# Performance work log

Measured on AMD Instinct MI355X. Metric: run time of the kernel, lower is better.

Reference implementation:

```python
import jax, jax.numpy as jnp
import numpy as np

B, N, F, G = 2, 8, 32, 32
EPS = 1e-8
elu = jax.nn.elu

def pconv(x, w, b):
    # pointwise Conv3d (1x1x1): x (..., C, D, H, W), w (O, C), b (O,)
    return jnp.einsum('...cdhw,oc->...odhw', x, w) + b[:, None, None, None]

def mean_var(x, weight):
    # weighted mean/variance over the num_images axis (axis=1), keepdims
    mean = jnp.sum(x * weight, axis=1, keepdims=True)
    var = jnp.sum(weight * (x - mean) ** 2, axis=1, keepdims=True)
    return mean, var

def setup_inputs() -> dict:
    key = jax.random.key(0)
    ks = jax.random.split(key, 20)
    def wmat(k, o, i):
        return jax.random.normal(k, (o, i), jnp.float32) * (1.0 / np.sqrt(i))
    return {
        'features': jax.random.normal(ks[0], (B, N, F, G, G, G), jnp.float32),
        'mask': jax.random.uniform(ks[1], (B, N, 1, G, G, G), jnp.float32),
        'voxel_depth': jax.random.normal(ks[2], (B, N, 1, G, G, G), jnp.float32),
        'voxel_dir': jax.random.normal(ks[3], (B, N, 3, G, G, G), jnp.float32),
        'rde_w1': wmat(ks[4], F // 2, 4), 'rde_b1': jnp.zeros((F // 2,), jnp.float32),
        'rde_w2': wmat(ks[5], F, F // 2), 'rde_b2': jnp.zeros((F,), jnp.float32),
        'base_w1': wmat(ks[6], 2 * F, 3 * F), 'base_b1': jnp.zeros((2 * F,), jnp.float32),
        'base_w2': wmat(ks[7], F, 2 * F), 'base_b2': jnp.zeros((F,), jnp.float32),
        'vis_w1': wmat(ks[8], F, F), 'vis_b1': jnp.zeros((F,), jnp.float32),
        'vis_w2': wmat(ks[9], F + 1, F), 'vis_b2': jnp.zeros((F + 1,), jnp.float32),
        'vis2_w1': wmat(ks[10], F, F), 'vis2_b1': jnp.zeros((F,), jnp.float32),
        'vis2_w2': wmat(ks[11], 1, F), 'vis2_b2': jnp.zeros((1,), jnp.float32),
        'stat_w': wmat(ks[12], F, 2 * F + 1), 'stat_b': jnp.zeros((F,), jnp.float32),
    }

def reference(features, mask, voxel_depth, voxel_dir,
              rde_w1, rde_b1, rde_w2, rde_b2,
              base_w1, base_b1, base_w2, base_b2,
              vis_w1, vis_b1, vis_w2, vis_b2,
              vis2_w1, vis2_b1, vis2_w2, vis2_b2,
              stat_w, stat_b):
    b, n = features.shape[:2]
    # ray/depth encoder (pointwise MLP over 4 channels)
    rde = jnp.concatenate([voxel_dir, voxel_depth], axis=2)  # (B,N,4,G,G,G)
    rde = elu(pconv(elu(pconv(rde, rde_w1, rde_b1)), rde_w2, rde_b2))
    feats = features + rde
    # mask-normalized weights over views
    weight = mask / (jnp.sum(mask, axis=1, keepdims=True) + EPS)
    mean, var = mean_var(feats, weight)
    gf = jnp.concatenate([mean, var], axis=2)  # (B,1,2F,G,G,G)
    x = jnp.concatenate([jnp.broadcast_to(gf, (b, n) + gf.shape[2:]), feats], axis=2)  # (B,N,3F,...)
    x = elu(pconv(elu(pconv(x, base_w1, base_b1)), base_w2, base_b2))
    xv = elu(pconv(elu(pconv(x * weight, vis_w1, vis_b1)), vis_w2, vis_b2))
    x_res, vis = xv[:, :, :-1], xv[:, :, -1:]
    vis = jax.nn.sigmoid(vis) * mask
    x = x + x_res
    vis = jax.nn.sigmoid(pconv(elu(pconv(x * vis, vis2_w1, vis2_b1)), vis2_w2, vis2_b2)) * mask
    weight = vis / (jnp.sum(vis, axis=1, keepdims=True) + EPS)
    mean, var = mean_var(x, weight)
    gf = jnp.concatenate([mean[:, 0], var[:, 0], jnp.mean(weight, axis=1)], axis=1)  # (B,2F+1,G,G,G)
    return elu(pconv(gf, stat_w, stat_b))  # (B,F,G,G,G)
```

## Files before the change

### kernel.cpp

```cpp
#include <hip/hip_runtime.h>


#define G3 32768
#define KP 104

typedef _Float16 h8 __attribute__((ext_vector_type(8)));
typedef _Float16 h4 __attribute__((ext_vector_type(4)));
typedef float f4 __attribute__((ext_vector_type(4)));

__device__ __forceinline__ float eluf(float x) {
    return x > 0.0f ? x : __expf(x) - 1.0f;
}
__device__ __forceinline__ float sigmoidf(float x) {
    return 1.0f / (1.0f + __expf(-x));
}

#define WS_BW1 0
#define WS_BW2 6144
#define WS_VW1 8192
#define WS_VW2 9216
#define WS_V2W1 10752
#define WS_H_TOT 11776
#define WS_VB2_BYTE (WS_H_TOT * 2)

__global__ void prep_kernel(const float* __restrict__ bw1,
                            const float* __restrict__ bw2,
                            const float* __restrict__ vw1,
                            const float* __restrict__ vw2,
                            const float* __restrict__ v2w1,
                            const float* __restrict__ vb2,
                            _Float16* __restrict__ wh,
                            float* __restrict__ vb2p) {
    int t = blockIdx.x * blockDim.x + threadIdx.x;
    int stride = gridDim.x * blockDim.x;
    for (int i = t; i < 6144; i += stride) wh[WS_BW1 + i] = (_Float16)bw1[i];
    for (int i = t; i < 2048; i += stride) wh[WS_BW2 + i] = (_Float16)bw2[i];
    for (int i = t; i < 1024; i += stride) wh[WS_VW1 + i] = (_Float16)vw1[i];
    for (int i = t; i < 1536; i += stride)
        wh[WS_VW2 + i] = (i < 1056) ? (_Float16)vw2[i] : (_Float16)0.0f;
    for (int i = t; i < 1024; i += stride) wh[WS_V2W1 + i] = (_Float16)v2w1[i];
    for (int i = t; i < 48; i += stride) vb2p[i] = (i < 33) ? vb2[i] : 0.0f;
}

template <int K, int KS, int MT>
__device__ __forceinline__ void mfma_tiles(const _Float16* __restrict__ Wf,
                                           const _Float16* __restrict__ Y,
                                           int srck0, int wave, int lane,
                                           f4 acc[2][4]) {
    const int q = lane >> 4, nlo = lane & 15;
#pragma unroll
    for (int j = 0; j < 2; ++j) {
        const int col = (wave + j * 4) * 16 + nlo;
        const _Float16* yc = Y + col * KP + srck0 + q * 8;
        h8 bf[KS];
#pragma unroll
        for (int kt = 0; kt < KS; ++kt) bf[kt] = *(const h8*)(yc + kt * 32);
#pragma unroll
        for (int mt = 0; mt < MT; ++mt) {
            f4 a = {0.f, 0.f, 0.f, 0.f};
            const _Float16* wr = Wf + (mt * 16 + nlo) * K + q * 8;
#pragma unroll
            for (int kt = 0; kt < KS; ++kt)
                a = __builtin_amdgcn_mfma_f32_16x16x32_f16(
                    *(const h8*)(wr + kt * 32), bf[kt], a, 0, 0, 0);
            acc[j][mt] = a;
        }
    }
}

template <int MT>
__device__ __forceinline__ void epi_store(f4 acc[2][4],
                                          const float* __restrict__ bias,
                                          _Float16* __restrict__ Y, int dstk0,
                                          int wave, int lane) {
    const int q = lane >> 4, nlo = lane & 15;
#pragma unroll
    for (int j = 0; j < 2; ++j) {
        const int col = (wave + j * 4) * 16 + nlo;
#pragma unroll
        for (int mt = 0; mt < MT; ++mt) {
            f4 bb = *(const f4*)(bias + mt * 16 + q * 4);
            f4 v = acc[j][mt];
            h4 hv;
#pragma unroll
            for (int r = 0; r < 4; ++r) hv[r] = (_Float16)eluf(v[r] + bb[r]);
            *(h4*)(Y + col * KP + dstk0 + mt * 16 + q * 4) = hv;
        }
    }
}

__global__ __launch_bounds__(256) void ibr_mfma(
    const float* __restrict__ features, const float* __restrict__ mask,
    const float* __restrict__ vdepth, const float* __restrict__ vdir,
    const float* __restrict__ rde_w1, const float* __restrict__ rde_b1,
    const float* __restrict__ rde_w2, const float* __restrict__ rde_b2,
    const float* __restrict__ base_b1, const float* __restrict__ base_b2,
    const float* __restrict__ vis_b1, const float* __restrict__ vis2_b1,
    const float* __restrict__ vis2_w2, const float* __restrict__ vis2_b2,
    const float* __restrict__ stat_w, const float* __restrict__ stat_b,
    const _Float16* __restrict__ wh, const float* __restrict__ vb2p,
    float* __restrict__ out) {
    __shared__ _Float16 Y[128 * KP];
    __shared__ float wtc[128], mval[128], visn_s[128], visv_s[128], wt2c[128];
    __shared__ float sA_v[16], wm_v[16];

    const int tid = threadIdx.x;
    const int lane = tid & 63;
    const int wave = tid >> 6;
    const int bb = blockIdx.x;
    const int b = bb >> 11;
    const int v0 = (bb & 2047) << 4;

    {
        const int n = tid >> 5, c = tid & 31;
        const float* fp = features + (((b * 8 + n) * 32 + c) << 15) + v0;
        f4 x0 = *(const f4*)(fp);
        f4 x1 = *(const f4*)(fp + 4);
        f4 x2 = *(const f4*)(fp + 8);
        f4 x3 = *(const f4*)(fp + 12);
        float va[16] = {x0[0], x0[1], x0[2], x0[3], x1[0], x1[1], x1[2], x1[3],
                        x2[0], x2[1], x2[2], x2[3], x3[0], x3[1], x3[2], x3[3]};
#pragma unroll
        for (int vi = 0; vi < 16; ++vi)
            Y[(vi * 8 + n) * KP + 64 + c] = (_Float16)va[vi];
    }
    if (tid < 128)
        mval[tid] = mask[((b * 8 + (tid & 7)) << 15) + v0 + (tid >> 3)];
    __syncthreads();

    if (tid < 128) {
        const int n = tid & 7, vi = tid >> 3, col = tid;
        const int bn = b * 8 + n, v = v0 + vi;
        const float r0 = vdir[(bn * 3 + 0) * G3 + v];
        const float r1 = vdir[(bn * 3 + 1) * G3 + v];
        const float r2 = vdir[(bn * 3 + 2) * G3 + v];
        const float r3 = vdepth[bn * G3 + v];
        float h16[16];
#pragma unroll
        for (int o = 0; o < 16; ++o) {
            float a = rde_b1[o] + rde_w1[o * 4 + 0] * r0 +
                      rde_w1[o * 4 + 1] * r1 + rde_w1[o * 4 + 2] * r2 +
                      rde_w1[o * 4 + 3] * r3;
            h16[o] = eluf(a);
        }
        float msum = 0.f;
#pragma unroll
        for (int k = 0; k < 8; ++k) msum += mval[vi * 8 + k];
        const float inv = 1.0f / (msum + 1e-8f);
        wtc[col] = mval[col] * inv;
        if (n == 0) sA_v[vi] = msum * inv;

        _Float16* yc = Y + col * KP + 64;
#pragma unroll
        for (int og = 0; og < 4; ++og) {
            h8 cur = *(h8*)(yc + og * 8);
#pragma unroll
            for (int oo = 0; oo < 8; ++oo) {
                const int o = og * 8 + oo;
                float a = rde_b2[o];
#pragma unroll
                for (int c = 0; c < 16; ++c) a += rde_w2[o * 16 + c] * h16[c];
                cur[oo] = (_Float16)((float)cur[oo] + eluf(a));
            }
            *(h8*)(yc + og * 8) = cur;
        }
    }
    __syncthreads();

#pragma unroll
    for (int t2 = 0; t2 < 2; ++t2) {
        const int idx = tid * 2 + t2;
        const int vi = idx >> 5, c = idx & 31;
        float s = 0.f, s2 = 0.f;
#pragma unroll
        for (int n = 0; n < 8; ++n) {
            const int col = vi * 8 + n;
            const float xv = (float)Y[col * KP + 64 + c];
            const float p = wtc[col] * xv;
            s += p;
            s2 += p * xv;
        }
        const float var = s2 - s * s * (2.0f - sA_v[vi]);
        const _Float16 hm = (_Float16)s, hva = (_Float16)var;
#pragma unroll
        for (int n = 0; n < 8; ++n) {
            Y[(vi * 8 + n) * KP + c] = hm;
            Y[(vi * 8 + n) * KP + 32 + c] = hva;
        }
    }
    __syncthreads();

    {
        f4 acc[2][4];
        mfma_tiles<96, 3, 4>(wh + WS_BW1, Y, 0, wave, lane, acc);
        __syncthreads();
        epi_store<4>(acc, base_b1, Y, 0, wave, lane);
    }
    __syncthreads();

    {
        f4 acc[2][4];
        mfma_tiles<64, 2, 2>(wh + WS_BW2, Y, 0, wave, lane, acc);
        __syncthreads();
        const int q = lane >> 4, nlo = lane & 15;
#pragma unroll
        for (int j = 0; j < 2; ++j) {
            const int col = (wave + j * 4) * 16 + nlo;
            const float wt = wtc[col];
#pragma unroll
            for (int mt = 0; mt < 2; ++mt) {
                f4 bbv = *(const f4*)(base_b2 + mt * 16 + q * 4);
                f4 v = acc[j][mt];
                h4 hx, hxw;
#pragma unroll
                for (int r = 0; r < 4; ++r) {
                    const float xv = eluf(v[r] + bbv[r]);
                    hx[r] = (_Float16)xv;
                    hxw[r] = (_Float16)(xv * wt);
                }
                *(h4*)(Y + col * KP + 64 + mt * 16 + q * 4) = hx;
                *(h4*)(Y + col * KP + mt * 16 + q * 4) = hxw;
            }
        }
    }
    __syncthreads();

    {
        f4 acc[2][4];
        mfma_tiles<32, 1, 2>(wh + WS_VW1, Y, 0, wave, lane, acc);
        __syncthreads();
        epi_store<2>(acc, vis_b1, Y, 32, wave, lane);
    }
    __syncthreads();

    {
        f4 acc[2][4];
        mfma_tiles<32, 1, 3>(wh + WS_VW2, Y, 32, wave, lane, acc);
        __syncthreads();
        const int q = lane >> 4, nlo = lane & 15;
#pragma unroll
        for (int j = 0; j < 2; ++j) {
            const int col = (wave + j * 4) * 16 + nlo;
#pragma unroll
            for (int mt = 0; mt < 2; ++mt) {
                f4 bbv = *(const f4*)(vb2p + mt * 16 + q * 4);
                f4 v = acc[j][mt];
                h4 hv;
#pragma unroll
                for (int r = 0; r < 4; ++r)
                    hv[r] = (_Float16)eluf(v[r] + bbv[r]);
                *(h4*)(Y + col * KP + mt * 16 + q * 4) = hv;
            }
            if (q == 0) {
                const float vv = acc[j][2][0] + vb2p[32];
                visn_s[col] = sigmoidf(eluf(vv)) * mval[col];
            }
        }
    }
    __syncthreads();

#pragma unroll
    for (int i = 0; i < 16; ++i) {
        const int idx = tid * 16 + i;
        const int col = idx >> 5, c = idx & 31;
        const float xr = (float)Y[col * KP + c];
        const float xo = (float)Y[col * KP + 64 + c];
        const float xn = xo + xr;
        Y[col * KP + 64 + c] = (_Float16)xn;
        Y[col * KP + c] = (_Float16)(xn * visn_s[col]);
    }
    __syncthreads();

    {
        f4 acc[2][4];
        mfma_tiles<32, 1, 2>(wh + WS_V2W1, Y, 0, wave, lane, acc);
        __syncthreads();
        epi_store<2>(acc, vis2_b1, Y, 32, wave, lane);
    }
    __syncthreads();

    if (tid < 128) {
        const int col = tid;
        const _Float16* yc = Y + col * KP + 32;
        float a0 = vis2_b2[0], a1 = 0.f, a2 = 0.f, a3 = 0.f;
#pragma unroll
        for (int c = 0; c < 32; c += 4) {
            a0 += vis2_w2[c + 0] * (float)yc[c + 0];
            a1 += vis2_w2[c + 1] * (float)yc[c + 1];
            a2 += vis2_w2[c + 2] * (float)yc[c + 2];
            a3 += vis2_w2[c + 3] * (float)yc[c + 3];
        }
        visv_s[col] = sigmoidf((a0 + a1) + (a2 + a3)) * mval[col];
    }
    __syncthreads();
    if (tid < 128) {
        const int vi = tid >> 3, n = tid & 7, col = tid;
        float b0 = 0.f;
#pragma unroll
        for (int k = 0; k < 8; ++k) b0 += visv_s[vi * 8 + k];
        const float inv = 1.0f / (b0 + 1e-8f);
        wt2c[col] = visv_s[col] * inv;
        if (n == 0) wm_v[vi] = b0 * inv * 0.125f;
    }
    __syncthreads();

#pragma unroll
    for (int t2 = 0; t2 < 2; ++t2) {
        const int idx = tid * 2 + t2;
        const int vi = idx >> 5, c = idx & 31;
        float s = 0.f, s2 = 0.f;
#pragma unroll
        for (int n = 0; n < 8; ++n) {
            const int col = vi * 8 + n;
            const float xv = (float)Y[col * KP + 64 + c];
            const float p = wt2c[col] * xv;
            s += p;
            s2 += p * xv;
        }
        const float sC = wm_v[vi] * 8.0f;
        const float var = s2 - s * s * (2.0f - sC);
        Y[(vi * 8) * KP + c] = (_Float16)s;
        Y[(vi * 8) * KP + 32 + c] = (_Float16)var;
    }
    __syncthreads();

    {
        const int vi = tid >> 4;
        const int o0 = (tid & 15) * 2;
        const _Float16* ym = Y + (vi * 8) * KP;
        const float wm = wm_v[vi];
#pragma unroll
        for (int jo = 0; jo < 2; ++jo) {
            const int o = o0 + jo;
            const float* row = stat_w + o * 65;
            float a0 = 0.f, a1 = 0.f, a2 = 0.f, a3 = 0.f;
#pragma unroll
            for (int c = 0; c < 32; c += 4) {
                a0 += row[c + 0] * (float)ym[c + 0];
                a1 += row[c + 1] * (float)ym[c + 1];
                a2 += row[c + 2] * (float)ym[c + 2];
                a3 += row[c + 3] * (float)ym[c + 3];
            }
#pragma unroll
            for (int c = 0; c < 32; c += 4) {
                a0 += row[32 + c + 0] * (float)ym[32 + c + 0];
                a1 += row[32 + c + 1] * (float)ym[32 + c + 1];
                a2 += row[32 + c + 2] * (float)ym[32 + c + 2];
                a3 += row[32 + c + 3] * (float)ym[32 + c + 3];
            }
            float a = (a0 + a1) + (a2 + a3) + row[64] * wm + stat_b[o];
            out[((b * 32 + o) << 15) + v0 + vi] = eluf(a);
        }
    }
}

extern "C" void kernel_launch(void* const* d_in, const int* in_sizes, int n_in,
                              void* d_out, int out_size, void* d_ws,
                              size_t ws_size, hipStream_t stream) {
    const float* features = (const float*)d_in[0];
    const float* mask = (const float*)d_in[1];
    const float* vdepth = (const float*)d_in[2];
    const float* vdir = (const float*)d_in[3];
    const float* rde_w1 = (const float*)d_in[4];
    const float* rde_b1 = (const float*)d_in[5];
    const float* rde_w2 = (const float*)d_in[6];
    const float* rde_b2 = (const float*)d_in[7];
    const float* base_w1 = (const float*)d_in[8];
    const float* base_b1 = (const float*)d_in[9];
    const float* base_w2 = (const float*)d_in[10];
    const float* base_b2 = (const float*)d_in[11];
    const float* vis_w1 = (const float*)d_in[12];
    const float* vis_b1 = (const float*)d_in[13];
    const float* vis_w2 = (const float*)d_in[14];
    const float* vis_b2 = (const float*)d_in[15];
    const float* vis2_w1 = (const float*)d_in[16];
    const float* vis2_b1 = (const float*)d_in[17];
    const float* vis2_w2 = (const float*)d_in[18];
    const float* vis2_b2 = (const float*)d_in[19];
    const float* stat_w = (const float*)d_in[20];
    const float* stat_b = (const float*)d_in[21];

    _Float16* wh = (_Float16*)d_ws;
    float* vb2p = (float*)((char*)d_ws + WS_VB2_BYTE);

    prep_kernel<<<24, 256, 0, stream>>>(base_w1, base_w2, vis_w1, vis_w2,
                                        vis2_w1, vis_b2, wh, vb2p);

    ibr_mfma<<<4096, 256, 0, stream>>>(
        features, mask, vdepth, vdir, rde_w1, rde_b1, rde_w2, rde_b2, base_b1,
        base_b2, vis_b1, vis2_b1, vis2_w2, vis2_b2, stat_w, stat_b, wh, vb2p,
        (float*)d_out);
}
```

Baseline: 243.4 us.

## Halve block tile to 8 voxels, drop prep kernel, convert fp32 weights in-kernel

```diff
diff --git a/kernel.cpp b/kernel.cpp
--- a/kernel.cpp
+++ b/kernel.cpp
@@ -6,7 +6,9 @@
 
 typedef _Float16 h8 __attribute__((ext_vector_type(8)));
 typedef _Float16 h4 __attribute__((ext_vector_type(4)));
+typedef _Float16 h2 __attribute__((ext_vector_type(2)));
 typedef float f4 __attribute__((ext_vector_type(4)));
+typedef float f2 __attribute__((ext_vector_type(2)));
 
 __device__ __forceinline__ float eluf(float x) {
     return x > 0.0f ? x : __expf(x) - 1.0f;
@@ -14,57 +16,52 @@
 __device__ __forceinline__ float sigmoidf(float x) {
     return 1.0f / (1.0f + __expf(-x));
 }
-
-#define WS_BW1 0
-#define WS_BW2 6144
-#define WS_VW1 8192
-#define WS_VW2 9216
-#define WS_V2W1 10752
-#define WS_H_TOT 11776
-#define WS_VB2_BYTE (WS_H_TOT * 2)
-
-__global__ void prep_kernel(const float* __restrict__ bw1,
-                            const float* __restrict__ bw2,
-                            const float* __restrict__ vw1,
-                            const float* __restrict__ vw2,
-                            const float* __restrict__ v2w1,
-                            const float* __restrict__ vb2,
-                            _Float16* __restrict__ wh,
-                            float* __restrict__ vb2p) {
-    int t = blockIdx.x * blockDim.x + threadIdx.x;
-    int stride = gridDim.x * blockDim.x;
-    for (int i = t; i < 6144; i += stride) wh[WS_BW1 + i] = (_Float16)bw1[i];
-    for (int i = t; i < 2048; i += stride) wh[WS_BW2 + i] = (_Float16)bw2[i];
-    for (int i = t; i < 1024; i += stride) wh[WS_VW1 + i] = (_Float16)vw1[i];
-    for (int i = t; i < 1536; i += stride)
-        wh[WS_VW2 + i] = (i < 1056) ? (_Float16)vw2[i] : (_Float16)0.0f;
-    for (int i = t; i < 1024; i += stride) wh[WS_V2W1 + i] = (_Float16)v2w1[i];
-    for (int i = t; i < 48; i += stride) vb2p[i] = (i < 33) ? vb2[i] : 0.0f;
+__device__ __forceinline__ h8 h8zero() {
+    h8 r;
+#pragma unroll
+    for (int i = 0; i < 8; ++i) r[i] = (_Float16)0.0f;
+    return r;
+}
+__device__ __forceinline__ h8 afrag_f32(const float* __restrict__ p) {
+    f4 x0 = *(const f4*)(p);
+    f4 x1 = *(const f4*)(p + 4);
+    h8 r;
+    r[0] = (_Float16)x0[0]; r[1] = (_Float16)x0[1];
+    r[2] = (_Float16)x0[2]; r[3] = (_Float16)x0[3];
+    r[4] = (_Float16)x1[0]; r[5] = (_Float16)x1[1];
+    r[6] = (_Float16)x1[2]; r[7] = (_Float16)x1[3];
+    return r;
 }
 
 template <int K, int KS, int MT>
-__device__ __forceinline__ void mfma_tiles(const _Float16* __restrict__ Wf,
+__device__ __forceinline__ void mfma_layer(const float* __restrict__ W,
                                            const _Float16* __restrict__ Y,
-                                           int srck0, int wave, int lane,
-                                           f4 acc[2][4]) {
+                                           int srck0, int rowlim, int wave,
+                                           int lane, f4 acc[2][4]) {
     const int q = lane >> 4, nlo = lane & 15;
+    h8 bf[2][KS];
 #pragma unroll
     for (int j = 0; j < 2; ++j) {
-        const int col = (wave + j * 4) * 16 + nlo;
+        const int col = (wave * 2 + j) * 16 + nlo;
         const _Float16* yc = Y + col * KP + srck0 + q * 8;
-        h8 bf[KS];
-#pragma unroll
-        for (int kt = 0; kt < KS; ++kt) bf[kt] = *(const h8*)(yc + kt * 32);
-#pragma unroll
-        for (int mt = 0; mt < MT; ++mt) {
-            f4 a = {0.f, 0.f, 0.f, 0.f};
-            const _Float16* wr = Wf + (mt * 16 + nlo) * K + q * 8;
+#pragma unroll
+        for (int kt = 0; kt < KS; ++kt) bf[j][kt] = *(const h8*)(yc + kt * 32);
+    }
+#pragma unroll
+    for (int mt = 0; mt < MT; ++mt) {
+        const int row = mt * 16 + nlo;
+        h8 af[KS];
+#pragma unroll
+        for (int kt = 0; kt < KS; ++kt)
+            af[kt] = (row < rowlim)
+                         ? afrag_f32(W + row * K + q * 8 + kt * 32)
+                         : h8zero();
+#pragma unroll
+        for (int j = 0; j < 2; ++j)
 #pragma unroll
             for (int kt = 0; kt < KS; ++kt)
-                a = __builtin_amdgcn_mfma_f32_16x16x32_f16(
-                    *(const h8*)(wr + kt * 32), bf[kt], a, 0, 0, 0);
-            acc[j][mt] = a;
-        }
+                acc[j][mt] = __builtin_amdgcn_mfma_f32_16x16x32_f16(
+                    af[kt], bf[j][kt], acc[j][mt], 0, 0, 0);
     }
 }
 
@@ -76,7 +73,7 @@
     const int q = lane >> 4, nlo = lane & 15;
 #pragma unroll
     for (int j = 0; j < 2; ++j) {
-        const int col = (wave + j * 4) * 16 + nlo;
+        const int col = (wave * 2 + j) * 16 + nlo;
 #pragma unroll
         for (int mt = 0; mt < MT; ++mt) {
             f4 bb = *(const f4*)(bias + mt * 16 + q * 4);
@@ -89,47 +86,57 @@
     }
 }
 
-__global__ __launch_bounds__(256) void ibr_mfma(
+__global__ __launch_bounds__(128) void ibr_mfma(
     const float* __restrict__ features, const float* __restrict__ mask,
     const float* __restrict__ vdepth, const float* __restrict__ vdir,
     const float* __restrict__ rde_w1, const float* __restrict__ rde_b1,
     const float* __restrict__ rde_w2, const float* __restrict__ rde_b2,
-    const float* __restrict__ base_b1, const float* __restrict__ base_b2,
-    const float* __restrict__ vis_b1, const float* __restrict__ vis2_b1,
+    const float* __restrict__ base_w1, const float* __restrict__ base_b1,
+    const float* __restrict__ base_w2, const float* __restrict__ base_b2,
+    const float* __restrict__ vis_w1, const float* __restrict__ vis_b1,
+    const float* __restrict__ vis_w2, const float* __restrict__ vis_b2,
+    const float* __restrict__ vis2_w1, const float* __restrict__ vis2_b1,
     const float* __restrict__ vis2_w2, const float* __restrict__ vis2_b2,
     const float* __restrict__ stat_w, const float* __restrict__ stat_b,
-    const _Float16* __restrict__ wh, const float* __restrict__ vb2p,
     float* __restrict__ out) {
-    __shared__ _Float16 Y[128 * KP];
-    __shared__ float wtc[128], mval[128], visn_s[128], visv_s[128], wt2c[128];
-    __shared__ float sA_v[16], wm_v[16];
+    __shared__ _Float16 Y[64 * KP];
+    __shared__ float stats[8 * 66];
+    __shared__ float mval[64], wtc[64], visn_s[64], visv_s[64], wt2c[64];
+    __shared__ float sA_v[8], wm_v[8];
 
     const int tid = threadIdx.x;
     const int lane = tid & 63;
     const int wave = tid >> 6;
     const int bb = blockIdx.x;
-    const int b = bb >> 11;
-    const int v0 = (bb & 2047) << 4;
-
-    {
-        const int n = tid >> 5, c = tid & 31;
-        const float* fp = features + (((b * 8 + n) * 32 + c) << 15) + v0;
-        f4 x0 = *(const f4*)(fp);
-        f4 x1 = *(const f4*)(fp + 4);
-        f4 x2 = *(const f4*)(fp + 8);
-        f4 x3 = *(const f4*)(fp + 12);
-        float va[16] = {x0[0], x0[1], x0[2], x0[3], x1[0], x1[1], x1[2], x1[3],
-                        x2[0], x2[1], x2[2], x2[3], x3[0], x3[1], x3[2], x3[3]};
-#pragma unroll
-        for (int vi = 0; vi < 16; ++vi)
-            Y[(vi * 8 + n) * KP + 64 + c] = (_Float16)va[vi];
-    }
-    if (tid < 128)
+    const int b = bb >> 12;
+    const int i = bb & 4095;
+    const int v0 = (((i & 7) << 9) | (i >> 3)) << 3;
+
+    {
+        const int n = tid >> 4;
+        const int cp = (tid & 15) * 2;
+        const float* fp0 = features + (((b * 8 + n) * 32 + cp) << 15) + v0;
+        f4 a0 = *(const f4*)(fp0);
+        f4 a1 = *(const f4*)(fp0 + 4);
+        f4 b0v = *(const f4*)(fp0 + G3);
+        f4 b1v = *(const f4*)(fp0 + G3 + 4);
+        float ca[8] = {a0[0], a0[1], a0[2], a0[3], a1[0], a1[1], a1[2], a1[3]};
+        float cb[8] = {b0v[0], b0v[1], b0v[2], b0v[3],
+                       b1v[0], b1v[1], b1v[2], b1v[3]};
+#pragma unroll
+        for (int vi = 0; vi < 8; ++vi) {
+            h2 t2 = {(_Float16)ca[vi], (_Float16)cb[vi]};
+            *(h2*)(Y + (vi * 8 + n) * KP + 64 + cp) = t2;
+        }
+    }
+    if (tid < 64)
         mval[tid] = mask[((b * 8 + (tid & 7)) << 15) + v0 + (tid >> 3)];
     __syncthreads();
 
-    if (tid < 128) {
-        const int n = tid & 7, vi = tid >> 3, col = tid;
+    {
+        const int col = tid & 63;
+        const int half = tid >> 6;
+        const int n = col & 7, vi = col >> 3;
         const int bn = b * 8 + n, v = v0 + vi;
         const float r0 = vdir[(bn * 3 + 0) * G3 + v];
         const float r1 = vdir[(bn * 3 + 1) * G3 + v];
@@ -143,20 +150,21 @@
                       rde_w1[o * 4 + 3] * r3;
             h16[o] = eluf(a);
         }
-        float msum = 0.f;
-#pragma unroll
-        for (int k = 0; k < 8; ++k) msum += mval[vi * 8 + k];
-        const float inv = 1.0f / (msum + 1e-8f);
-        wtc[col] = mval[col] * inv;
-        if (n == 0) sA_v[vi] = msum * inv;
-
-        _Float16* yc = Y + col * KP + 64;
-#pragma unroll
-        for (int og = 0; og < 4; ++og) {
+        if (half == 0) {
+            float msum = 0.f;
+#pragma unroll
+            for (int k = 0; k < 8; ++k) msum += mval[vi * 8 + k];
+            const float inv = 1.0f / (msum + 1e-8f);
+            wtc[col] = mval[col] * inv;
+            if (n == 0) sA_v[vi] = msum * inv;
+        }
+        _Float16* yc = Y + col * KP + 64 + half * 16;
+#pragma unroll
+        for (int og = 0; og < 2; ++og) {
             h8 cur = *(h8*)(yc + og * 8);
 #pragma unroll
             for (int oo = 0; oo < 8; ++oo) {
-                const int o = og * 8 + oo;
+                const int o = half * 16 + og * 8 + oo;
                 float a = rde_b2[o];
 #pragma unroll
                 for (int c = 0; c < 16; ++c) a += rde_w2[o * 16 + c] * h16[c];
@@ -167,45 +175,45 @@
     }
     __syncthreads();
 
-#pragma unroll
-    for (int t2 = 0; t2 < 2; ++t2) {
-        const int idx = tid * 2 + t2;
-        const int vi = idx >> 5, c = idx & 31;
-        float s = 0.f, s2 = 0.f;
+    {
+        const int vi = tid >> 4, cp = (tid & 15) * 2;
+        float s0 = 0.f, s1 = 0.f, q0 = 0.f, q1 = 0.f;
 #pragma unroll
         for (int n = 0; n < 8; ++n) {
             const int col = vi * 8 + n;
-            const float xv = (float)Y[col * KP + 64 + c];
-            const float p = wtc[col] * xv;
-            s += p;
-            s2 += p * xv;
-        }
-        const float var = s2 - s * s * (2.0f - sA_v[vi]);
-        const _Float16 hm = (_Float16)s, hva = (_Float16)var;
+            h2 xv = *(const h2*)(Y + col * KP + 64 + cp);
+            const float wv = wtc[col];
+            const float x0 = (float)xv[0], x1 = (float)xv[1];
+            s0 += wv * x0; q0 += wv * x0 * x0;
+            s1 += wv * x1; q1 += wv * x1 * x1;
+        }
+        const float k = 2.0f - sA_v[vi];
+        h2 hm = {(_Float16)s0, (_Float16)s1};
+        h2 hv = {(_Float16)(q0 - s0 * s0 * k), (_Float16)(q1 - s1 * s1 * k)};
 #pragma unroll
         for (int n = 0; n < 8; ++n) {
-            Y[(vi * 8 + n) * KP + c] = hm;
-            Y[(vi * 8 + n) * KP + 32 + c] = hva;
-        }
-    }
-    __syncthreads();
-
-    {
-        f4 acc[2][4];
-        mfma_tiles<96, 3, 4>(wh + WS_BW1, Y, 0, wave, lane, acc);
+            *(h2*)(Y + (vi * 8 + n) * KP + cp) = hm;
+            *(h2*)(Y + (vi * 8 + n) * KP + 32 + cp) = hv;
+        }
+    }
+    __syncthreads();
+
+    {
+        f4 acc[2][4] = {};
+        mfma_layer<96, 3, 4>(base_w1, Y, 0, 1 << 30, wave, lane, acc);
         __syncthreads();
         epi_store<4>(acc, base_b1, Y, 0, wave, lane);
     }
     __syncthreads();
 
     {
-        f4 acc[2][4];
-        mfma_tiles<64, 2, 2>(wh + WS_BW2, Y, 0, wave, lane, acc);
+        f4 acc[2][4] = {};
+        mfma_layer<64, 2, 2>(base_w2, Y, 0, 1 << 30, wave, lane, acc);
         __syncthreads();
         const int q = lane >> 4, nlo = lane & 15;
 #pragma unroll
         for (int j = 0; j < 2; ++j) {
-            const int col = (wave + j * 4) * 16 + nlo;
+            const int col = (wave * 2 + j) * 16 + nlo;
             const float wt = wtc[col];
 #pragma unroll
             for (int mt = 0; mt < 2; ++mt) {
@@ -226,24 +234,22 @@
     __syncthreads();
 
     {
-        f4 acc[2][4];
-        mfma_tiles<32, 1, 2>(wh + WS_VW1, Y, 0, wave, lane, acc);
-        __syncthreads();
+        f4 acc[2][4] = {};
+        mfma_layer<32, 1, 2>(vis_w1, Y, 0, 1 << 30, wave, lane, acc);
         epi_store<2>(acc, vis_b1, Y, 32, wave, lane);
     }
     __syncthreads();
 
     {
-        f4 acc[2][4];
-        mfma_tiles<32, 1, 3>(wh + WS_VW2, Y, 32, wave, lane, acc);
-        __syncthreads();
+        f4 acc[2][4] = {};
+        mfma_layer<32, 1, 3>(vis_w2, Y, 32, 33, wave, lane, acc);
         const int q = lane >> 4, nlo = lane & 15;
 #pragma unroll
         for (int j = 0; j < 2; ++j) {
-            const int col = (wave + j * 4) * 16 + nlo;
+            const int col = (wave * 2 + j) * 16 + nlo;
 #pragma unroll
             for (int mt = 0; mt < 2; ++mt) {
-                f4 bbv = *(const f4*)(vb2p + mt * 16 + q * 4);
+                f4 bbv = *(const f4*)(vis_b2 + mt * 16 + q * 4);
                 f4 v = acc[j][mt];
                 h4 hv;
 #pragma unroll
@@ -252,105 +258,103 @@
                 *(h4*)(Y + col * KP + mt * 16 + q * 4) = hv;
             }
             if (q == 0) {
-                const float vv = acc[j][2][0] + vb2p[32];
+                const float vv = acc[j][2][0] + vis_b2[32];
                 visn_s[col] = sigmoidf(eluf(vv)) * mval[col];
             }
         }
     }
     __syncthreads();
 
-#pragma unroll
-    for (int i = 0; i < 16; ++i) {
-        const int idx = tid * 16 + i;
-        const int col = idx >> 5, c = idx & 31;
-        const float xr = (float)Y[col * KP + c];
-        const float xo = (float)Y[col * KP + 64 + c];
-        const float xn = xo + xr;
-        Y[col * KP + 64 + c] = (_Float16)xn;
-        Y[col * KP + c] = (_Float16)(xn * visn_s[col]);
-    }
-    __syncthreads();
-
-    {
-        f4 acc[2][4];
-        mfma_tiles<32, 1, 2>(wh + WS_V2W1, Y, 0, wave, lane, acc);
-        __syncthreads();
+    {
+        const int n = tid >> 4, cp = (tid & 15) * 2;
+#pragma unroll
+        for (int vi = 0; vi < 8; ++vi) {
+            const int col = vi * 8 + n;
+            h2 xr = *(const h2*)(Y + col * KP + cp);
+            h2 xo = *(const h2*)(Y + col * KP + 64 + cp);
+            const float vn = visn_s[col];
+            const float x0 = (float)xo[0] + (float)xr[0];
+            const float x1 = (float)xo[1] + (float)xr[1];
+            h2 hx = {(_Float16)x0, (_Float16)x1};
+            h2 hxv = {(_Float16)(x0 * vn), (_Float16)(x1 * vn)};
+            *(h2*)(Y + col * KP + 64 + cp) = hx;
+            *(h2*)(Y + col * KP + cp) = hxv;
+        }
+    }
+    __syncthreads();
+
+    {
+        f4 acc[2][4] = {};
+        mfma_layer<32, 1, 2>(vis2_w1, Y, 0, 1 << 30, wave, lane, acc);
         epi_store<2>(acc, vis2_b1, Y, 32, wave, lane);
     }
     __syncthreads();
 
-    if (tid < 128) {
-        const int col = tid;
-        const _Float16* yc = Y + col * KP + 32;
-        float a0 = vis2_b2[0], a1 = 0.f, a2 = 0.f, a3 = 0.f;
+    if (tid < 64) {
+        const _Float16* yc = Y + tid * KP + 32;
+        float a0 = vis2_b2[0], a1 = 0.f;
 #pragma unroll
         for (int c = 0; c < 32; c += 4) {
-            a0 += vis2_w2[c + 0] * (float)yc[c + 0];
-            a1 += vis2_w2[c + 1] * (float)yc[c + 1];
-            a2 += vis2_w2[c + 2] * (float)yc[c + 2];
-            a3 += vis2_w2[c + 3] * (float)yc[c + 3];
-        }
-        visv_s[col] = sigmoidf((a0 + a1) + (a2 + a3)) * mval[col];
-    }
-    __syncthreads();
-    if (tid < 128) {
-        const int vi = tid >> 3, n = tid & 7, col = tid;
+            h2 p0 = *(const h2*)(yc + c);
+            h2 p1 = *(const h2*)(yc + c + 2);
+            a0 += vis2_w2[c + 0] * (float)p0[0] + vis2_w2[c + 1] * (float)p0[1];
+            a1 += vis2_w2[c + 2] * (float)p1[0] + vis2_w2[c + 3] * (float)p1[1];
+        }
+        visv_s[tid] = sigmoidf(a0 + a1) * mval[tid];
+    }
+    __syncthreads();
+    if (tid < 64) {
+        const int vi = tid >> 3, n = tid & 7;
         float b0 = 0.f;
 #pragma unroll
         for (int k = 0; k < 8; ++k) b0 += visv_s[vi * 8 + k];
         const float inv = 1.0f / (b0 + 1e-8f);
-        wt2c[col] = visv_s[col] * inv;
+        wt2c[tid] = visv_s[tid] * inv;
         if (n == 0) wm_v[vi] = b0 * inv * 0.125f;
     }
     __syncthreads();
 
-#pragma unroll
-    for (int t2 = 0; t2 < 2; ++t2) {
-        const int idx = tid * 2 + t2;
-        const int vi = idx >> 5, c = idx & 31;
-        float s = 0.f, s2 = 0.f;
+    {
+        const int vi = tid >> 4, cp = (tid & 15) * 2;
+        float s0 = 0.f, s1 = 0.f, q0 = 0.f, q1 = 0.f;
 #pragma unroll
         for (int n = 0; n < 8; ++n) {
             const int col = vi * 8 + n;
-            const float xv = (float)Y[col * KP + 64 + c];
-            const float p = wt2c[col] * xv;
-            s += p;
-            s2 += p * xv;
+            h2 xv = *(const h2*)(Y + col * KP + 64 + cp);
+            const float wv = wt2c[col];
+            const float x0 = (float)xv[0], x1 = (float)xv[1];
+            s0 += wv * x0; q0 += wv * x0 * x0;
+            s1 += wv * x1; q1 += wv * x1 * x1;
         }
         const float sC = wm_v[vi] * 8.0f;
-        const float var = s2 - s * s * (2.0f - sC);
-        Y[(vi * 8) * KP + c] = (_Float16)s;
-        Y[(vi * 8) * KP + 32 + c] = (_Float16)var;
-    }
-    __syncthreads();
-
-    {
-        const int vi = tid >> 4;
-        const int o0 = (tid & 15) * 2;
-        const _Float16* ym = Y + (vi * 8) * KP;
-        const float wm = wm_v[vi];
-#pragma unroll
-        for (int jo = 0; jo < 2; ++jo) {
-            const int o = o0 + jo;
-            const float* row = stat_w + o * 65;
-            float a0 = 0.f, a1 = 0.f, a2 = 0.f, a3 = 0.f;
-#pragma unroll
-            for (int c = 0; c < 32; c += 4) {
-                a0 += row[c + 0] * (float)ym[c + 0];
-                a1 += row[c + 1] * (float)ym[c + 1];
-                a2 += row[c + 2] * (float)ym[c + 2];
-                a3 += row[c + 3] * (float)ym[c + 3];
-            }
-#pragma unroll
-            for (int c = 0; c < 32; c += 4) {
-                a0 += row[32 + c + 0] * (float)ym[32 + c + 0];
-                a1 += row[32 + c + 1] * (float)ym[32 + c + 1];
-                a2 += row[32 + c + 2] * (float)ym[32 + c + 2];
-                a3 += row[32 + c + 3] * (float)ym[32 + c + 3];
-            }
-            float a = (a0 + a1) + (a2 + a3) + row[64] * wm + stat_b[o];
-            out[((b * 32 + o) << 15) + v0 + vi] = eluf(a);
-        }
+        const float k = 2.0f - sC;
+        f2 mpair = {s0, s1};
+        f2 vpair = {q0 - s0 * s0 * k, q1 - s1 * s1 * k};
+        *(f2*)(stats + vi * 66 + cp) = mpair;
+        *(f2*)(stats + vi * 66 + 32 + cp) = vpair;
+        if (cp == 0) stats[vi * 66 + 64] = wm_v[vi];
+    }
+    __syncthreads();
+
+    {
+        const int o = tid >> 2;
+        const int vi0 = (tid & 3) * 2;
+        const float* row = stat_w + o * 65;
+        const float* sa = stats + vi0 * 66;
+        const float* sb = stats + (vi0 + 1) * 66;
+        float p0 = stat_b[o], p1 = p0, p2 = 0.f, p3 = 0.f;
+#pragma unroll
+        for (int c = 0; c < 32; c += 2) {
+            const float w0 = row[c], w1 = row[c + 1];
+            const float u0 = row[32 + c], u1 = row[32 + c + 1];
+            p0 += w0 * sa[c] + u0 * sa[32 + c];
+            p2 += w1 * sa[c + 1] + u1 * sa[32 + c + 1];
+            p1 += w0 * sb[c] + u0 * sb[32 + c];
+            p3 += w1 * sb[c + 1] + u1 * sb[32 + c + 1];
+        }
+        const float wlast = row[64];
+        f2 r = {eluf(p0 + p2 + wlast * sa[64]), eluf(p1 + p3 + wlast * sb[64])};
+        *(f2*)(out + ((b * 32 + o) << 15) + v0 + vi0) = r;
     }
 }
 
@@ -380,14 +384,8 @@
     const float* stat_w = (const float*)d_in[20];
     const float* stat_b = (const float*)d_in[21];
 
-    _Float16* wh = (_Float16*)d_ws;
-    float* vb2p = (float*)((char*)d_ws + WS_VB2_BYTE);
-
-    prep_kernel<<<24, 256, 0, stream>>>(base_w1, base_w2, vis_w1, vis_w2,
-                                        vis2_w1, vis_b2, wh, vb2p);
-
-    ibr_mfma<<<4096, 256, 0, stream>>>(
-        features, mask, vdepth, vdir, rde_w1, rde_b1, rde_w2, rde_b2, base_b1,
-        base_b2, vis_b1, vis2_b1, vis2_w2, vis2_b2, stat_w, stat_b, wh, vb2p,
-        (float*)d_out);
-}
+    ibr_mfma<<<8192, 128, 0, stream>>>(
+        features, mask, vdepth, vdir, rde_w1, rde_b1, rde_w2, rde_b2, base_w1,
+        base_b1, base_w2, base_b2, vis_w1, vis_b1, vis_w2, vis_b2, vis2_w1,
+        vis2_b1, vis2_w2, vis2_b2, stat_w, stat_b, (float*)d_out);
+}
```

Result: slower. 287.6 us (+18.1%).
